# Kernel tuning notes

Measured on AMD Instinct MI355X. Metric: run time of the kernel, lower is better.

## Reference

```python
import jax, jax.numpy as jnp
import numpy as np

N1, N2, D = 8192, 8192, 128

def setup_inputs() -> dict:
    key = jax.random.key(0)
    k1, k2 = jax.random.split(key)
    desc1 = jax.random.normal(k1, (N1, D), dtype=jnp.float32)
    desc2 = jax.random.normal(k2, (N2, D), dtype=jnp.float32)
    return {"desc1": desc1, "desc2": desc2}

def reference(desc1, desc2):
    # sim: [N1, N2] descriptor similarity matrix
    sim = desc1 @ desc2.T
    # mutual nearest-neighbor matching ('nnm' mode)
    nn12 = jnp.argmax(sim, axis=1)            # [N1] best match in image 2 for each kp in image 1
    nn21 = jnp.argmax(sim, axis=0)            # [N2] best match in image 1 for each kp in image 2
    ids1 = jnp.arange(sim.shape[0])
    mutual = nn21[nn12] == ids1               # mutual-consistency check
    # dense jit-friendly encoding of the ragged match list: -1 where no mutual match
    matches0 = jnp.where(mutual, nn12, -1)    # [N1] int
    # matching_scores0 = top-1 similarity per row (torch.topk(..., k=1)[0].squeeze())
    scores = jnp.max(sim, axis=1)             # [N1]
    return matches0, scores
```

## Files before the change

kernel.cpp:

```cpp
#include <hip/hip_runtime.h>
#include <stdint.h>

#define N1 8192
#define N2 8192
#define DK 128
#define TAU 0.08f
#define BIAS 256.0f
#define LDR 132

typedef _Float16 half8 __attribute__((ext_vector_type(8)));
typedef _Float16 half4 __attribute__((ext_vector_type(4)));
typedef float floatx4 __attribute__((ext_vector_type(4)));

__device__ __align__(16) _Float16 g_Af[N1 * DK];
__device__ __align__(16) _Float16 g_Bf[N2 * DK];
__device__ __align__(16) float2 g_rowtop2[64 * N1];
__device__ __align__(16) float2 g_coltop2[64 * N2];
__device__ int g_nn12[N1];
__device__ int g_nn21[N2];

__device__ __forceinline__ float bval(float key) {
    return __uint_as_float(__float_as_uint(key) & 0xFFFFFF80u);
}
__device__ __forceinline__ int bidx(float key) {
    return (int)(__float_as_uint(key) & 127u);
}
__device__ __forceinline__ void push2f(float& t1, float& t2, float p) {
    float m = __builtin_amdgcn_fmed3f(t1, t2, p);
    t1 = fmaxf(t1, p);
    t2 = m;
}
__device__ __forceinline__ void merge2f(float& t1, float& t2, float o1, float o2) {
    float x = fmaxf(t2, o2);
    float m = __builtin_amdgcn_fmed3f(t1, o1, x);
    t1 = fmaxf(t1, o1);
    t2 = m;
}
__device__ __forceinline__ float2 m2(float2 a, float2 b) {
    merge2f(a.x, a.y, b.x, b.y);
    return a;
}
#define DPPF(x, ctrl) __int_as_float(__builtin_amdgcn_update_dpp( \
        0, __float_as_int(x), (ctrl), 0xF, 0xF, true))

__device__ __forceinline__ unsigned mono32(float v) {
    unsigned u = __float_as_uint(v);
    return u ^ ((u & 0x80000000u) ? 0xFFFFFFFFu : 0x80000000u);
}
__device__ __forceinline__ float unmono32(unsigned k) {
    unsigned u = (k & 0x80000000u) ? (k ^ 0x80000000u) : ~k;
    return __uint_as_float(u);
}
__device__ __forceinline__ unsigned long long pack64(float d, unsigned idx) {
    return ((unsigned long long)mono32(d) << 32) | (unsigned)(~idx);
}

__global__ __launch_bounds__(256) void convert_kernel(const float* __restrict__ A,
                                                      const float* __restrict__ B) {
    int t = blockIdx.x * blockDim.x + threadIdx.x;
    const int perMat = N1 * (DK / 4);
    int which = (t >= perMat) ? 1 : 0;
    const float* src = which ? B : A;
    _Float16* dst = which ? g_Bf : g_Af;
    int i = which ? t - perMat : t;
    int m = i >> 5;
    int kq = i & 31;
    float4 v = *reinterpret_cast<const float4*>(src + (size_t)m * DK + kq * 4);
    half4 h = {(_Float16)v.x, (_Float16)v.y, (_Float16)v.z, (_Float16)v.w};
    *reinterpret_cast<half4*>(dst + (size_t)m * DK + kq * 4) = h;
}

__global__ __launch_bounds__(256) void simf16_kernel() {
    __shared__ union {
        _Float16 Bs[128 * LDR];
        float2 scr[128][34];
    } sm;
    __shared__ float2 lmerge[2][128];

    const int tid  = threadIdx.x;
    const int lane = tid & 63;
    const int wave = tid >> 6;
    const int wm = wave >> 1, wn = wave & 1;
    const int fr = lane & 15, q = lane >> 4;

    const int flat = blockIdx.y * 64 + blockIdx.x;
    const int xcd = flat & 7;
    const int j = flat >> 3;
    const int ty = j >> 3;
    const int tx = ((j & 7) << 3) | xcd;
    const int row0 = ty * 128, col0 = tx * 128;

#pragma unroll
    for (int i = 0; i < 8; ++i) {
        int f = i * 256 + tid;
        int r = f >> 4, c = f & 15;
        *reinterpret_cast<float4*>(&sm.Bs[r * LDR + c * 8]) =
            *reinterpret_cast<const float4*>(g_Bf + (size_t)(col0 + r) * DK + c * 8);
    }

    floatx4 acc[4][4];
#pragma unroll
    for (int mt = 0; mt < 4; ++mt)
#pragma unroll
        for (int nt = 0; nt < 4; ++nt)
            acc[mt][nt] = (floatx4){0.f, 0.f, 0.f, 0.f};

    const _Float16* Abase = g_Af + (size_t)(row0 + wm * 64 + fr) * DK + q * 8;

    half8 af[4], afn[4];
#pragma unroll
    for (int mt = 0; mt < 4; ++mt)
        af[mt] = *reinterpret_cast<const half8*>(Abase + mt * 16 * DK);

    __syncthreads();

#pragma unroll
    for (int ks = 0; ks < 4; ++ks) {
        if (ks < 3) {
#pragma unroll
            for (int mt = 0; mt < 4; ++mt)
                afn[mt] = *reinterpret_cast<const half8*>(Abase + mt * 16 * DK + (ks + 1) * 32);
        }
        half8 bf[4];
#pragma unroll
        for (int nt = 0; nt < 4; ++nt)
            bf[nt] = *reinterpret_cast<const half8*>(&sm.Bs[(wn * 64 + nt * 16 + fr) * LDR + ks * 32 + q * 8]);
        __builtin_amdgcn_s_setprio(1);
#pragma unroll
        for (int mt = 0; mt < 4; ++mt)
#pragma unroll
            for (int nt = 0; nt < 4; ++nt)
                acc[mt][nt] = __builtin_amdgcn_mfma_f32_16x16x32_f16(af[mt], bf[nt], acc[mt][nt], 0, 0, 0);
        __builtin_amdgcn_s_setprio(0);
        if (ks < 3) {
#pragma unroll
            for (int mt = 0; mt < 4; ++mt)
                af[mt] = afn[mt];
        }
    }

#pragma unroll
    for (int mt = 0; mt < 4; ++mt)
#pragma unroll
        for (int nt = 0; nt < 4; ++nt)
#pragma unroll
            for (int reg = 0; reg < 4; ++reg)
                acc[mt][nt][reg] = __uint_as_float(
                    __float_as_uint(acc[mt][nt][reg] + BIAS) & 0xFFFFFF80u);

#pragma unroll
    for (int nt = 0; nt < 4; ++nt) {
        float t1 = 0.f, t2 = 0.f;
#pragma unroll
        for (int mt = 0; mt < 4; ++mt)
#pragma unroll
            for (int reg = 0; reg < 4; ++reg)
                push2f(t1, t2, __uint_as_float(__float_as_uint(acc[mt][nt][reg])
                                               | (unsigned)(wm * 64 + mt * 16 + q * 4 + reg)));
        float o1 = __shfl_xor(t1, 16, 64), o2 = __shfl_xor(t2, 16, 64);
        merge2f(t1, t2, o1, o2);
        o1 = __shfl_xor(t1, 32, 64); o2 = __shfl_xor(t2, 32, 64);
        merge2f(t1, t2, o1, o2);
        if (q == 0) lmerge[wm][wn * 64 + nt * 16 + fr] = make_float2(t1, t2);
    }

    __syncthreads();

#pragma unroll
    for (int mt = 0; mt < 4; ++mt) {
#pragma unroll
        for (int reg = 0; reg < 4; ++reg) {
            float t1 = 0.f, t2 = 0.f;
#pragma unroll
            for (int nt = 0; nt < 4; ++nt)
                push2f(t1, t2, __uint_as_float(__float_as_uint(acc[mt][nt][reg])
                                               | (unsigned)(wn * 64 + nt * 16 + fr)));
            sm.scr[wm * 64 + mt * 16 + q * 4 + reg][wn * 16 + fr] = make_float2(t1, t2);
        }
    }

    if (tid < 128) {
        float2 a = lmerge[0][tid], b = lmerge[1][tid];
        merge2f(a.x, a.y, b.x, b.y);
        g_coltop2[(size_t)ty * N2 + col0 + tid] = a;
    }
    __syncthreads();

    {
        const int row = tid >> 1, h = tid & 1;
        const float4* p = reinterpret_cast<const float4*>(&sm.scr[row][h * 16]);
        float4 v0 = p[0], v1 = p[1], v2 = p[2], v3 = p[3];
        float4 v4 = p[4], v5 = p[5], v6 = p[6], v7 = p[7];
        float2 r0 = m2(make_float2(v0.x, v0.y), make_float2(v0.z, v0.w));
        float2 r1 = m2(make_float2(v1.x, v1.y), make_float2(v1.z, v1.w));
        float2 r2 = m2(make_float2(v2.x, v2.y), make_float2(v2.z, v2.w));
        float2 r3 = m2(make_float2(v3.x, v3.y), make_float2(v3.z, v3.w));
        float2 r4 = m2(make_float2(v4.x, v4.y), make_float2(v4.z, v4.w));
        float2 r5 = m2(make_float2(v5.x, v5.y), make_float2(v5.z, v5.w));
        float2 r6 = m2(make_float2(v6.x, v6.y), make_float2(v6.z, v6.w));
        float2 r7 = m2(make_float2(v7.x, v7.y), make_float2(v7.z, v7.w));
        r0 = m2(r0, r1); r2 = m2(r2, r3); r4 = m2(r4, r5); r6 = m2(r6, r7);
        r0 = m2(r0, r2); r4 = m2(r4, r6);
        r0 = m2(r0, r4);
        float o1 = __shfl_xor(r0.x, 1, 64), o2 = __shfl_xor(r0.y, 1, 64);
        merge2f(r0.x, r0.y, o1, o2);
        if (h == 0) g_rowtop2[(size_t)tx * N1 + row0 + row] = r0;
    }
}

__global__ __launch_bounds__(256) void fix_kernel(const float* __restrict__ A,
                                                  const float* __restrict__ B,
                                                  float* __restrict__ out) {
    __shared__ float2 tile[64 * 16];
    __shared__ unsigned long long slot[16];
    __shared__ int cand[256];
    __shared__ int cand_cnt;

    const int tid = threadIdx.x;
    const bool rowside = blockIdx.x >= 512;
    const int base0 = (blockIdx.x & 511) * 16;
    const float2* top2 = rowside ? g_rowtop2 : g_coltop2;

#pragma unroll
    for (int i = 0; i < 4; ++i) {
        int idx = i * 256 + tid;
        int grp = idx >> 4, c = idx & 15;
        tile[grp * 16 + c] = top2[(size_t)grp * N1 + base0 + c];
    }
    if (tid < 16) slot[tid] = 0ULL;
    if (tid == 0) cand_cnt = 0;
    __syncthreads();

    const int c = tid >> 4, j = tid & 15;
    float mx = 0.f;
#pragma unroll
    for (int s = 0; s < 4; ++s)
        mx = fmaxf(mx, tile[(j * 4 + s) * 16 + c].x);
    mx = fmaxf(mx, DPPF(mx, 0xB1));
    mx = fmaxf(mx, DPPF(mx, 0x4E));
    mx = fmaxf(mx, DPPF(mx, 0x124));
    mx = fmaxf(mx, DPPF(mx, 0x128));
    const float thr = bval(mx) - TAU;
#pragma unroll
    for (int s = 0; s < 4; ++s) {
        int grp = j * 4 + s;
        float2 e = tile[grp * 16 + c];
        if (bval(e.x) >= thr) {
            int o = grp * 128 + bidx(e.x);
            int si = atomicAdd(&cand_cnt, 1);
            if (si < 256) cand[si] = (c << 16) | o;
        }
        if (bval(e.y) >= thr) {
            int o = grp * 128 + bidx(e.y);
            int si = atomicAdd(&cand_cnt, 1);
            if (si < 256) cand[si] = (c << 16) | o;
        }
    }
    __syncthreads();

    const int nc = min(cand_cnt, 256);
    for (int i = tid; i < nc; i += 256) {
        int pc = cand[i];
        int cl = pc >> 16, other = pc & 0xFFFF;
        const float* ar = rowside ? (A + (size_t)(base0 + cl) * DK) : (A + (size_t)other * DK);
        const float* br = rowside ? (B + (size_t)other * DK) : (B + (size_t)(base0 + cl) * DK);
        float d = 0.0f;
#pragma unroll
        for (int k4 = 0; k4 < DK / 4; ++k4) {
            float4 a = *reinterpret_cast<const float4*>(ar + k4 * 4);
            float4 b = *reinterpret_cast<const float4*>(br + k4 * 4);
            d = fmaf(a.x, b.x, d);
            d = fmaf(a.y, b.y, d);
            d = fmaf(a.z, b.z, d);
            d = fmaf(a.w, b.w, d);
        }
        atomicMax(&slot[cl], pack64(d, (unsigned)other));
    }
    __syncthreads();

    if (tid < 16) {
        unsigned long long p = slot[tid];
        int idx = base0 + tid;
        if (rowside) {
            g_nn12[idx] = (int)(~(unsigned)p);
            out[N1 + idx] = unmono32((unsigned)(p >> 32));
        } else {
            g_nn21[idx] = (int)(~(unsigned)p);
        }
    }
}

__global__ __launch_bounds__(256) void mutual_kernel(float* __restrict__ out) {
    int i = blockIdx.x * blockDim.x + threadIdx.x;
    if (i < N1) {
        int m = g_nn12[i];
        out[i] = (float)((g_nn21[m] == i) ? m : -1);
    }
}

extern "C" void kernel_launch(void* const* d_in, const int* in_sizes, int n_in,
                              void* d_out, int out_size, void* d_ws, size_t ws_size,
                              hipStream_t stream) {
    const float* A = (const float*)d_in[0];
    const float* B = (const float*)d_in[1];
    float* out = (float*)d_out;

    convert_kernel<<<2 * N1 * (DK / 4) / 256, 256, 0, stream>>>(A, B);
    dim3 grid(64, 64);
    simf16_kernel<<<grid, 256, 0, stream>>>();
    fix_kernel<<<1024, 256, 0, stream>>>(A, B, out);
    mutual_kernel<<<N1 / 256, 256, 0, stream>>>(out);
}
```

Measured before the change: 111.4 us.

## Split 128x128 similarity tile across eight waves with smaller per-wave accumulators

```diff
diff --git a/kernel.cpp b/kernel.cpp
--- a/kernel.cpp
+++ b/kernel.cpp
@@ -70,7 +70,7 @@
     *reinterpret_cast<half4*>(dst + (size_t)m * DK + kq * 4) = h;
 }
 
-__global__ __launch_bounds__(256) void simf16_kernel() {
+__global__ __launch_bounds__(512) void simf16_kernel() {
     __shared__ union {
         _Float16 Bs[128 * LDR];
         float2 scr[128][34];
@@ -80,7 +80,7 @@
     const int tid  = threadIdx.x;
     const int lane = tid & 63;
     const int wave = tid >> 6;
-    const int wm = wave >> 1, wn = wave & 1;
+    const int wm = wave >> 2, wn = wave & 3;
     const int fr = lane & 15, q = lane >> 4;
 
     const int flat = blockIdx.y * 64 + blockIdx.x;
@@ -91,65 +91,52 @@
     const int row0 = ty * 128, col0 = tx * 128;
 
 #pragma unroll
-    for (int i = 0; i < 8; ++i) {
-        int f = i * 256 + tid;
+    for (int i = 0; i < 4; ++i) {
+        int f = i * 512 + tid;
         int r = f >> 4, c = f & 15;
         *reinterpret_cast<float4*>(&sm.Bs[r * LDR + c * 8]) =
             *reinterpret_cast<const float4*>(g_Bf + (size_t)(col0 + r) * DK + c * 8);
     }
 
-    floatx4 acc[4][4];
+    floatx4 acc[4][2];
 #pragma unroll
     for (int mt = 0; mt < 4; ++mt)
 #pragma unroll
-        for (int nt = 0; nt < 4; ++nt)
+        for (int nt = 0; nt < 2; ++nt)
             acc[mt][nt] = (floatx4){0.f, 0.f, 0.f, 0.f};
 
     const _Float16* Abase = g_Af + (size_t)(row0 + wm * 64 + fr) * DK + q * 8;
 
-    half8 af[4], afn[4];
+    __syncthreads();
+
+#pragma unroll
+    for (int ks = 0; ks < 4; ++ks) {
+        half8 af[4];
+#pragma unroll
+        for (int mt = 0; mt < 4; ++mt)
+            af[mt] = *reinterpret_cast<const half8*>(Abase + mt * 16 * DK + ks * 32);
+        half8 bf0 = *reinterpret_cast<const half8*>(&sm.Bs[(wn * 32 + fr) * LDR + ks * 32 + q * 8]);
+        half8 bf1 = *reinterpret_cast<const half8*>(&sm.Bs[(wn * 32 + 16 + fr) * LDR + ks * 32 + q * 8]);
+        __builtin_amdgcn_s_setprio(1);
+#pragma unroll
+        for (int mt = 0; mt < 4; ++mt) {
+            acc[mt][0] = __builtin_amdgcn_mfma_f32_16x16x32_f16(af[mt], bf0, acc[mt][0], 0, 0, 0);
+            acc[mt][1] = __builtin_amdgcn_mfma_f32_16x16x32_f16(af[mt], bf1, acc[mt][1], 0, 0, 0);
+        }
+        __builtin_amdgcn_s_setprio(0);
+    }
+
 #pragma unroll
     for (int mt = 0; mt < 4; ++mt)
-        af[mt] = *reinterpret_cast<const half8*>(Abase + mt * 16 * DK);
-
-    __syncthreads();
-
-#pragma unroll
-    for (int ks = 0; ks < 4; ++ks) {
-        if (ks < 3) {
-#pragma unroll
-            for (int mt = 0; mt < 4; ++mt)
-                afn[mt] = *reinterpret_cast<const half8*>(Abase + mt * 16 * DK + (ks + 1) * 32);
-        }
-        half8 bf[4];
-#pragma unroll
-        for (int nt = 0; nt < 4; ++nt)
-            bf[nt] = *reinterpret_cast<const half8*>(&sm.Bs[(wn * 64 + nt * 16 + fr) * LDR + ks * 32 + q * 8]);
-        __builtin_amdgcn_s_setprio(1);
-#pragma unroll
-        for (int mt = 0; mt < 4; ++mt)
-#pragma unroll
-            for (int nt = 0; nt < 4; ++nt)
-                acc[mt][nt] = __builtin_amdgcn_mfma_f32_16x16x32_f16(af[mt], bf[nt], acc[mt][nt], 0, 0, 0);
-        __builtin_amdgcn_s_setprio(0);
-        if (ks < 3) {
-#pragma unroll
-            for (int mt = 0; mt < 4; ++mt)
-                af[mt] = afn[mt];
-        }
-    }
-
-#pragma unroll
-    for (int mt = 0; mt < 4; ++mt)
-#pragma unroll
-        for (int nt = 0; nt < 4; ++nt)
+#pragma unroll
+        for (int nt = 0; nt < 2; ++nt)
 #pragma unroll
             for (int reg = 0; reg < 4; ++reg)
                 acc[mt][nt][reg] = __uint_as_float(
                     __float_as_uint(acc[mt][nt][reg] + BIAS) & 0xFFFFFF80u);
 
 #pragma unroll
-    for (int nt = 0; nt < 4; ++nt) {
+    for (int nt = 0; nt < 2; ++nt) {
         float t1 = 0.f, t2 = 0.f;
 #pragma unroll
         for (int mt = 0; mt < 4; ++mt)
@@ -161,7 +148,7 @@
         merge2f(t1, t2, o1, o2);
         o1 = __shfl_xor(t1, 32, 64); o2 = __shfl_xor(t2, 32, 64);
         merge2f(t1, t2, o1, o2);
-        if (q == 0) lmerge[wm][wn * 64 + nt * 16 + fr] = make_float2(t1, t2);
+        if (q == 0) lmerge[wm][wn * 32 + nt * 16 + fr] = make_float2(t1, t2);
     }
 
     __syncthreads();
@@ -171,11 +158,15 @@
 #pragma unroll
         for (int reg = 0; reg < 4; ++reg) {
             float t1 = 0.f, t2 = 0.f;
-#pragma unroll
-            for (int nt = 0; nt < 4; ++nt)
-                push2f(t1, t2, __uint_as_float(__float_as_uint(acc[mt][nt][reg])
-                                               | (unsigned)(wn * 64 + nt * 16 + fr)));
-            sm.scr[wm * 64 + mt * 16 + q * 4 + reg][wn * 16 + fr] = make_float2(t1, t2);
+            push2f(t1, t2, __uint_as_float(__float_as_uint(acc[mt][0][reg])
+                                           | (unsigned)(wn * 32 + fr)));
+            push2f(t1, t2, __uint_as_float(__float_as_uint(acc[mt][1][reg])
+                                           | (unsigned)(wn * 32 + 16 + fr)));
+            float o1 = __shfl_xor(t1, 8, 64), o2 = __shfl_xor(t2, 8, 64);
+            merge2f(t1, t2, o1, o2);
+            if ((lane & 8) == 0)
+                sm.scr[wm * 64 + mt * 16 + q * 4 + reg][wn * 8 + (fr & 7)] =
+                    make_float2(t1, t2);
         }
     }
 
@@ -187,22 +178,18 @@
     __syncthreads();
 
     {
-        const int row = tid >> 1, h = tid & 1;
-        const float4* p = reinterpret_cast<const float4*>(&sm.scr[row][h * 16]);
+        const int row = tid >> 2, h = tid & 3;
+        const float4* p = reinterpret_cast<const float4*>(&sm.scr[row][h * 8]);
         float4 v0 = p[0], v1 = p[1], v2 = p[2], v3 = p[3];
-        float4 v4 = p[4], v5 = p[5], v6 = p[6], v7 = p[7];
         float2 r0 = m2(make_float2(v0.x, v0.y), make_float2(v0.z, v0.w));
         float2 r1 = m2(make_float2(v1.x, v1.y), make_float2(v1.z, v1.w));
         float2 r2 = m2(make_float2(v2.x, v2.y), make_float2(v2.z, v2.w));
         float2 r3 = m2(make_float2(v3.x, v3.y), make_float2(v3.z, v3.w));
-        float2 r4 = m2(make_float2(v4.x, v4.y), make_float2(v4.z, v4.w));
-        float2 r5 = m2(make_float2(v5.x, v5.y), make_float2(v5.z, v5.w));
-        float2 r6 = m2(make_float2(v6.x, v6.y), make_float2(v6.z, v6.w));
-        float2 r7 = m2(make_float2(v7.x, v7.y), make_float2(v7.z, v7.w));
-        r0 = m2(r0, r1); r2 = m2(r2, r3); r4 = m2(r4, r5); r6 = m2(r6, r7);
-        r0 = m2(r0, r2); r4 = m2(r4, r6);
-        r0 = m2(r0, r4);
+        r0 = m2(r0, r1); r2 = m2(r2, r3);
+        r0 = m2(r0, r2);
         float o1 = __shfl_xor(r0.x, 1, 64), o2 = __shfl_xor(r0.y, 1, 64);
+        merge2f(r0.x, r0.y, o1, o2);
+        o1 = __shfl_xor(r0.x, 2, 64); o2 = __shfl_xor(r0.y, 2, 64);
         merge2f(r0.x, r0.y, o1, o2);
         if (h == 0) g_rowtop2[(size_t)tx * N1 + row0 + row] = r0;
     }
@@ -307,7 +294,7 @@
 
     convert_kernel<<<2 * N1 * (DK / 4) / 256, 256, 0, stream>>>(A, B);
     dim3 grid(64, 64);
-    simf16_kernel<<<grid, 256, 0, stream>>>();
+    simf16_kernel<<<grid, 512, 0, stream>>>();
     fix_kernel<<<1024, 256, 0, stream>>>(A, B, out);
     mutual_kernel<<<N1 / 256, 256, 0, stream>>>(out);
 }
```

New measurement: 135.8 us. 21.9% more time.
